# Optimization experiments

Measured on AMD Instinct MI355X. Metric: run time of the kernel, lower is better.

Reference implementation:

```python
import jax, jax.numpy as jnp
import numpy as np

# Problem sizes (batched graph of G molecules)
N = 100_000   # total nodes
E = 400_000   # total directed edges
G = 2_500     # number of molecule graphs
K = 3         # len(idx_wo_smiles) -> zero rows inserted
NODE_F = 74   # graph_feats_shape[0]
EDGE_F = 12   # graph_feats_shape[1]
HID = 128     # hidden_feats = dim // 2
DIM = 256     # dim


def setup_inputs() -> dict:
    key = jax.random.key(0)
    ks = jax.random.split(key, 20)
    init = lambda k, shape, fan: (jax.random.normal(k, shape, jnp.float32) / np.sqrt(fan)).astype(jnp.float32)

    node_feats = jax.random.normal(ks[0], (N, NODE_F), jnp.float32)
    edge_feats = jax.random.normal(ks[1], (E, EDGE_F), jnp.float32)  # passed but unused by GCN
    src = jax.random.randint(ks[2], (E,), 0, N)
    dst = jax.random.randint(ks[3], (E,), 0, N)
    # sorted graph ids, every graph non-empty (~40 atoms each)
    graph_ids = (jnp.arange(N) * G) // N
    idx_wo_smiles = jnp.arange(K)

    return {
        'node_feats': node_feats,
        'edge_feats': edge_feats,
        'W1': init(ks[4], (NODE_F, HID), NODE_F), 'b1': jnp.zeros((HID,), jnp.float32),
        'Wr1': init(ks[5], (NODE_F, HID), NODE_F), 'br1': jnp.zeros((HID,), jnp.float32),
        'W2': init(ks[6], (HID, HID), HID), 'b2': jnp.zeros((HID,), jnp.float32),
        'Wr2': init(ks[7], (HID, HID), HID), 'br2': jnp.zeros((HID,), jnp.float32),
        'w_atom': init(ks[8], (HID, 1), HID), 'b_atom': jnp.zeros((1,), jnp.float32),
        'Wp1': init(ks[9], (2 * HID, HID), 2 * HID), 'bp1': jnp.zeros((HID,), jnp.float32),
        'Wp2': init(ks[10], (HID, DIM), HID), 'bp2': jnp.zeros((DIM,), jnp.float32),
        'src': src, 'dst': dst, 'graph_ids': graph_ids, 'idx_wo_smiles': idx_wo_smiles,
    }


def reference(node_feats, edge_feats, W1, b1, Wr1, br1, W2, b2, Wr2, br2,
              w_atom, b_atom, Wp1, bp1, Wp2, bp2, src, dst, graph_ids, idx_wo_smiles):
    n = node_feats.shape[0]
    ones_e = jnp.ones(src.shape[0], jnp.float32)
    out_deg = jax.ops.segment_sum(ones_e, src, num_segments=n)
    in_deg = jax.ops.segment_sum(ones_e, dst, num_segments=n)
    norm_s = jax.lax.rsqrt(jnp.maximum(out_deg, 1.0))  # [N]
    norm_d = jax.lax.rsqrt(jnp.maximum(in_deg, 1.0))   # [N]

    def gcn_layer(h, W, b, Wr, br):
        # GraphConv(norm='both'): D^-1/2 A D^-1/2 h W + b, with relu activation
        m = h[src] * norm_s[src][:, None]                       # [E, F] gather
        agg = jax.ops.segment_sum(m, dst, num_segments=n)       # [N, F] scatter-add
        gc = jax.nn.relu((agg * norm_d[:, None]) @ W + b)
        res = jax.nn.relu(h @ Wr + br)                          # residual connection
        return gc + res

    h = gcn_layer(node_feats, W1, b1, Wr1, br1)   # [N, HID]
    h = gcn_layer(h, W2, b2, Wr2, br2)            # [N, HID]

    # WeightedSumAndMax readout per molecule
    aw = jax.nn.sigmoid(h @ w_atom + b_atom)                          # [N, 1]
    hsum = jax.ops.segment_sum(h * aw, graph_ids, num_segments=G)     # [G, HID]
    hmax = jax.ops.segment_max(h, graph_ids, num_segments=G)          # [G, HID]
    gfeat = jnp.concatenate([hsum, hmax], axis=1)                     # [G, 2*HID]

    latent = jax.nn.relu(gfeat @ Wp1 + bp1) @ Wp2 + bp2               # [G, DIM]

    # Insert zero rows at idx_wo_smiles (sorted ascending -> final positions)
    total = G + idx_wo_smiles.shape[0]
    zero_mask = jnp.zeros((total,), bool).at[idx_wo_smiles].set(True)
    keep = jnp.nonzero(~zero_mask, size=G)[0]
    out = jnp.zeros((total, latent.shape[1]), latent.dtype).at[keep].set(latent)
    return out
```

## Files before the change

kernel.cpp:

```cpp
#include <hip/hip_runtime.h>
#include <hip/hip_bf16.h>

#define NODE_F 74
#define HID 128
#define DIM 256

typedef __hip_bfloat16 bf16;
typedef unsigned int u32;
typedef unsigned short u16;

typedef short s16x8 __attribute__((ext_vector_type(8)));
typedef __bf16 bf16x8 __attribute__((ext_vector_type(8)));
typedef float f32x4 __attribute__((ext_vector_type(4)));

__device__ __forceinline__ float rdl(float v, int l){
  return __int_as_float(__builtin_amdgcn_readlane(__float_as_int(v), l));
}
__device__ __forceinline__ float2 bfpair(u32 u){
  float2 r;
  r.x = __uint_as_float(u << 16);
  r.y = __uint_as_float(u & 0xffff0000u);
  return r;
}
__device__ __forceinline__ u16 bfbits(float a){
  return __bfloat16_as_ushort(__float2bfloat16(a));
}

__global__ void k_deg(const int* __restrict__ src, const int* __restrict__ dst,
                      float* __restrict__ outdeg_f, int* __restrict__ indeg, int E_){
  int e = blockIdx.x*256 + threadIdx.x;
  if (e < E_){
    atomicAdd(&outdeg_f[src[e]], 1.0f);
    atomicAdd(&indeg[dst[e]], 1);
  }
}

__global__ __launch_bounds__(256) void k_scan_a(const int* __restrict__ indeg,
                                                float* __restrict__ norm_s,
                                                float* __restrict__ norm_d,
                                                int* __restrict__ bsum, int n){
  __shared__ int red[256];
  const int base = blockIdx.x*1024 + threadIdx.x*4;
  int s = 0;
  #pragma unroll
  for (int i = 0; i < 4; ++i){
    const int idx = base + i;
    if (idx < n){
      const int d = indeg[idx];
      s += d;
      norm_d[idx] = rsqrtf(fmaxf((float)d, 1.0f));
      norm_s[idx] = rsqrtf(fmaxf(norm_s[idx], 1.0f));
    }
  }
  red[threadIdx.x] = s;
  __syncthreads();
  #pragma unroll
  for (int off = 128; off; off >>= 1){
    if (threadIdx.x < off) red[threadIdx.x] += red[threadIdx.x + off];
    __syncthreads();
  }
  if (threadIdx.x == 0) bsum[blockIdx.x] = red[0];
}

__global__ __launch_bounds__(1024) void k_scan_b(int* __restrict__ bsum, int nb){
  __shared__ int part[1024];
  __shared__ int carry;
  if (threadIdx.x == 0) carry = 0;
  __syncthreads();
  for (int c0 = 0; c0 < nb; c0 += 1024){
    const int tid = threadIdx.x, idx = c0 + tid;
    part[tid] = (idx < nb) ? bsum[idx] : 0;
    __syncthreads();
    for (int off = 1; off < 1024; off <<= 1){
      const int t = (tid >= off) ? part[tid-off] : 0;
      __syncthreads();
      part[tid] += t;
      __syncthreads();
    }
    if (idx < nb) bsum[idx] = carry + ((tid == 0) ? 0 : part[tid-1]);
    __syncthreads();
    if (tid == 0) carry += part[1023];
    __syncthreads();
  }
}

__global__ __launch_bounds__(256) void k_scan_c(int* __restrict__ indeg,
                                                const int* __restrict__ bsum,
                                                int* __restrict__ row_ptr, int n){
  __shared__ int part[256];
  const int base = blockIdx.x*1024 + threadIdx.x*4;
  int v[4]; int s = 0;
  #pragma unroll
  for (int i = 0; i < 4; ++i){
    const int idx = base + i;
    v[i] = (idx < n) ? indeg[idx] : 0;
    s += v[i];
  }
  part[threadIdx.x] = s;
  __syncthreads();
  for (int off = 1; off < 256; off <<= 1){
    const int t = (threadIdx.x >= off) ? part[threadIdx.x-off] : 0;
    __syncthreads();
    part[threadIdx.x] += t;
    __syncthreads();
  }
  int run = bsum[blockIdx.x] + ((threadIdx.x == 0) ? 0 : part[threadIdx.x-1]);
  #pragma unroll
  for (int i = 0; i < 4; ++i){
    const int idx = base + i;
    if (idx < n){
      row_ptr[idx] = run;
      run += v[i];
      indeg[idx] = 0;
    }
    if (idx == n-1) row_ptr[n] = run;
  }
}

__global__ void k_fill(const int* __restrict__ src, const int* __restrict__ dst,
                       const int* __restrict__ row_ptr, int* __restrict__ cursor,
                       int* __restrict__ col, int E_){
  int e = blockIdx.x*256 + threadIdx.x;
  if (e < E_){
    int d = dst[e];
    int pos = row_ptr[d] + atomicAdd(&cursor[d], 1);
    col[pos] = src[e];
  }
}

__global__ __launch_bounds__(256) void k_prep_all(
    const float* __restrict__ W1, const float* __restrict__ Wr1,
    const float* __restrict__ W2, const float* __restrict__ Wr2,
    u16* __restrict__ Bp1, u16* __restrict__ Bp2){
  int idx = blockIdx.x*256 + threadIdx.x;
  const float* W; u16* dst; int S, Ktrue, loc;
  if      (idx < 12288){ W = W1;  dst = Bp1;          S = 3; Ktrue = NODE_F; loc = idx; }
  else if (idx < 24576){ W = Wr1; dst = Bp1 + 12288;  S = 3; Ktrue = NODE_F; loc = idx - 12288; }
  else if (idx < 40960){ W = W2;  dst = Bp2;          S = 4; Ktrue = HID;    loc = idx - 24576; }
  else if (idx < 57344){ W = Wr2; dst = Bp2 + 16384;  S = 4; Ktrue = HID;    loc = idx - 40960; }
  else return;
  const int e   = loc & 7;
  const int l   = (loc >> 3) & 63;
  const int rem = loc >> 9;
  const int s   = rem % S;
  const int t   = rem / S;
  const int k   = s*32 + (l >> 4)*8 + e;
  const int c   = t*16 + (l & 15);
  const float v = (k < Ktrue) ? W[(size_t)k*HID + c] : 0.f;
  dst[loc] = bfbits(v);
}

__global__ __launch_bounds__(256) void k_fgemm1(
    const float* __restrict__ x0, const int* __restrict__ row_ptr,
    const int* __restrict__ col, const float* __restrict__ norm_s,
    const float* __restrict__ norm_d,
    const u16* __restrict__ Bp, const float* __restrict__ bg_,
    const float* __restrict__ br_, u16* __restrict__ h1, int n){
  const int lane = threadIdx.x & 63;
  const int wid  = threadIdx.x >> 6;
  const int jg = lane & 15, kg = lane >> 4;
  const int r0 = blockIdx.x*64 + wid*16;
  const int row = r0 + jg;
  const bool rok = row < n;
  const int kb = kg*8;

  float agg[3][8];
  #pragma unroll
  for (int s = 0; s < 3; ++s)
    #pragma unroll
    for (int e = 0; e < 8; ++e) agg[s][e] = 0.f;

  auto accum = [&](const float* px, float ns){
    #pragma unroll
    for (int s = 0; s < 2; ++s){
      #pragma unroll
      for (int e = 0; e < 8; e += 2){
        const float2 v = *(const float2*)&px[s*32 + kb + e];
        agg[s][e]   = fmaf(v.x, ns, agg[s][e]);
        agg[s][e+1] = fmaf(v.y, ns, agg[s][e+1]);
      }
    }
    if (kg == 0){
      #pragma unroll
      for (int e = 0; e < 8; e += 2){
        const float2 v = *(const float2*)&px[64 + e];
        agg[2][e]   = fmaf(v.x, ns, agg[2][e]);
        agg[2][e+1] = fmaf(v.y, ns, agg[2][e+1]);
      }
    } else if (kg == 1){
      const float2 v = *(const float2*)&px[72];
      agg[2][0] = fmaf(v.x, ns, agg[2][0]);
      agg[2][1] = fmaf(v.y, ns, agg[2][1]);
    }
  };

  int p0 = 0, p1 = 0;
  if (rok){ p0 = row_ptr[row]; p1 = row_ptr[row+1]; }
  int p = p0;
  #pragma unroll 1
  for (; p + 3 < p1; p += 4){
    const int s0 = col[p], s1 = col[p+1], s2 = col[p+2], s3 = col[p+3];
    const float n0 = norm_s[s0], n1 = norm_s[s1], n2 = norm_s[s2], n3 = norm_s[s3];
    accum(x0 + (size_t)s0*NODE_F, n0);
    accum(x0 + (size_t)s1*NODE_F, n1);
    accum(x0 + (size_t)s2*NODE_F, n2);
    accum(x0 + (size_t)s3*NODE_F, n3);
  }
  #pragma unroll 1
  for (; p + 1 < p1; p += 2){
    const int s0 = col[p], s1 = col[p+1];
    const float n0 = norm_s[s0], n1 = norm_s[s1];
    accum(x0 + (size_t)s0*NODE_F, n0);
    accum(x0 + (size_t)s1*NODE_F, n1);
  }
  if (p < p1){
    const int s0 = col[p];
    accum(x0 + (size_t)s0*NODE_F, norm_s[s0]);
  }

  const float nd = rok ? norm_d[row] : 0.f;
  bf16x8 ag[3], ar[3];
  #pragma unroll
  for (int s = 0; s < 3; ++s)
    #pragma unroll
    for (int e = 0; e < 8; ++e) ag[s][e] = (__bf16)(agg[s][e]*nd);

  {
    const int rA = rok ? row : (n-1);
    const float* px = x0 + (size_t)rA*NODE_F;
    #pragma unroll
    for (int s = 0; s < 2; ++s)
      #pragma unroll
      for (int e = 0; e < 8; e += 2){
        const float2 w = *(const float2*)&px[s*32 + kb + e];
        ar[s][e]   = (__bf16)w.x;
        ar[s][e+1] = (__bf16)w.y;
      }
    #pragma unroll
    for (int e = 0; e < 8; ++e) ar[2][e] = (__bf16)0.f;
    if (kg == 0){
      #pragma unroll
      for (int e = 0; e < 8; e += 2){
        const float2 w = *(const float2*)&px[64 + e];
        ar[2][e]   = (__bf16)w.x;
        ar[2][e+1] = (__bf16)w.y;
      }
    } else if (kg == 1){
      const float2 w = *(const float2*)&px[72];
      ar[2][0] = (__bf16)w.x;
      ar[2][1] = (__bf16)w.y;
    }
  }

  f32x4 accg[8], accr[8];
  #pragma unroll
  for (int t = 0; t < 8; ++t){
    accg[t] = f32x4{0.f,0.f,0.f,0.f};
    accr[t] = f32x4{0.f,0.f,0.f,0.f};
  }
  constexpr int FR1 = 8*3*512;
  #pragma unroll
  for (int s = 0; s < 3; ++s){
    #pragma unroll
    for (int t = 0; t < 8; ++t){
      const bf16x8 bg = __builtin_bit_cast(bf16x8,
          *(const s16x8*)&Bp[((t*3 + s)*64 + lane)*8]);
      const bf16x8 br = __builtin_bit_cast(bf16x8,
          *(const s16x8*)&Bp[FR1 + ((t*3 + s)*64 + lane)*8]);
      accg[t] = __builtin_amdgcn_mfma_f32_16x16x32_bf16(ag[s], bg, accg[t], 0,0,0);
      accr[t] = __builtin_amdgcn_mfma_f32_16x16x32_bf16(ar[s], br, accr[t], 0,0,0);
    }
  }

  const int rowb = r0 + 4*kg;
  #pragma unroll
  for (int t = 0; t < 8; ++t){
    const int colc = t*16 + jg;
    const float bgv = bg_[colc], brv = br_[colc];
    #pragma unroll
    for (int r = 0; r < 4; ++r){
      const int row2 = rowb + r;
      if (row2 < n){
        const float o = fmaxf(accg[t][r] + bgv, 0.f) + fmaxf(accr[t][r] + brv, 0.f);
        h1[(size_t)row2*HID + colc] = bfbits(o);
      }
    }
  }
}

__global__ __launch_bounds__(256) void k_fgemm2(
    const u16* __restrict__ h1, const int* __restrict__ row_ptr,
    const int* __restrict__ col, const float* __restrict__ norm_s,
    const float* __restrict__ norm_d,
    const u16* __restrict__ Bp, const float* __restrict__ bg_,
    const float* __restrict__ br_,
    const float* __restrict__ w_atom, const float* __restrict__ b_atom,
    const int* __restrict__ gid,
    float* __restrict__ hsum, u32* __restrict__ hmax, int n){
  const int lane = threadIdx.x & 63;
  const int wid  = threadIdx.x >> 6;
  const int jg = lane & 15, kg = lane >> 4;
  const int r0 = blockIdx.x*64 + wid*16;
  const int row = r0 + jg;
  const bool rok = row < n;
  const int kb = kg*8;

  float agg[4][8];
  #pragma unroll
  for (int s = 0; s < 4; ++s)
    #pragma unroll
    for (int e = 0; e < 8; ++e) agg[s][e] = 0.f;

  auto accum = [&](uint4 v, int s, float ns){
    const float2 f0 = bfpair(v.x), f1 = bfpair(v.y);
    const float2 f2 = bfpair(v.z), f3 = bfpair(v.w);
    agg[s][0] = fmaf(f0.x, ns, agg[s][0]);
    agg[s][1] = fmaf(f0.y, ns, agg[s][1]);
    agg[s][2] = fmaf(f1.x, ns, agg[s][2]);
    agg[s][3] = fmaf(f1.y, ns, agg[s][3]);
    agg[s][4] = fmaf(f2.x, ns, agg[s][4]);
    agg[s][5] = fmaf(f2.y, ns, agg[s][5]);
    agg[s][6] = fmaf(f3.x, ns, agg[s][6]);
    agg[s][7] = fmaf(f3.y, ns, agg[s][7]);
  };
  auto gatherN = [&](const u16* ph, float ns){
    const uint4 v0 = *(const uint4*)(ph);
    const uint4 v1 = *(const uint4*)(ph + 32);
    const uint4 v2 = *(const uint4*)(ph + 64);
    const uint4 v3 = *(const uint4*)(ph + 96);
    accum(v0, 0, ns); accum(v1, 1, ns); accum(v2, 2, ns); accum(v3, 3, ns);
  };

  int p0 = 0, p1 = 0;
  if (rok){ p0 = row_ptr[row]; p1 = row_ptr[row+1]; }
  int p = p0;
  #pragma unroll 1
  for (; p + 3 < p1; p += 4){
    const int s0 = col[p], s1 = col[p+1], s2 = col[p+2], s3 = col[p+3];
    const float n0 = norm_s[s0], n1 = norm_s[s1], n2 = norm_s[s2], n3 = norm_s[s3];
    gatherN(h1 + (size_t)s0*HID + kb, n0);
    gatherN(h1 + (size_t)s1*HID + kb, n1);
    gatherN(h1 + (size_t)s2*HID + kb, n2);
    gatherN(h1 + (size_t)s3*HID + kb, n3);
  }
  #pragma unroll 1
  for (; p + 1 < p1; p += 2){
    const int s0 = col[p], s1 = col[p+1];
    const float n0 = norm_s[s0], n1 = norm_s[s1];
    gatherN(h1 + (size_t)s0*HID + kb, n0);
    gatherN(h1 + (size_t)s1*HID + kb, n1);
  }
  if (p < p1){
    const int s0 = col[p];
    gatherN(h1 + (size_t)s0*HID + kb, norm_s[s0]);
  }

  const float nd = rok ? norm_d[row] : 0.f;
  bf16x8 ag[4];
  #pragma unroll
  for (int s = 0; s < 4; ++s)
    #pragma unroll
    for (int e = 0; e < 8; ++e) ag[s][e] = (__bf16)(agg[s][e]*nd);

  const int rA = rok ? row : (n-1);
  const u16* phr = h1 + (size_t)rA*HID + kb;

  f32x4 accg[8], accr[8];
  #pragma unroll
  for (int t = 0; t < 8; ++t){
    accg[t] = f32x4{0.f,0.f,0.f,0.f};
    accr[t] = f32x4{0.f,0.f,0.f,0.f};
  }
  constexpr int FR2 = 8*4*512;
  #pragma unroll
  for (int s = 0; s < 4; ++s){
    const bf16x8 arf = __builtin_bit_cast(bf16x8, *(const s16x8*)(phr + s*32));
    #pragma unroll
    for (int t = 0; t < 8; ++t){
      const bf16x8 bg = __builtin_bit_cast(bf16x8,
          *(const s16x8*)&Bp[((t*4 + s)*64 + lane)*8]);
      const bf16x8 br = __builtin_bit_cast(bf16x8,
          *(const s16x8*)&Bp[FR2 + ((t*4 + s)*64 + lane)*8]);
      accg[t] = __builtin_amdgcn_mfma_f32_16x16x32_bf16(ag[s], bg, accg[t], 0,0,0);
      accr[t] = __builtin_amdgcn_mfma_f32_16x16x32_bf16(arf, br, accr[t], 0,0,0);
    }
  }

  float o[8][4];
  #pragma unroll
  for (int t = 0; t < 8; ++t){
    const int colc = t*16 + jg;
    const float bgv = bg_[colc], brv = br_[colc];
    #pragma unroll
    for (int r = 0; r < 4; ++r)
      o[t][r] = fmaxf(accg[t][r] + bgv, 0.f) + fmaxf(accr[t][r] + brv, 0.f);
  }
  if (r0 < n){
    float wa[8];
    #pragma unroll
    for (int t = 0; t < 8; ++t) wa[t] = w_atom[t*16 + jg];
    const float ba = b_atom[0];
    const int rowb = r0 + 4*kg;
    float awv[4]; int gidr[4];
    #pragma unroll
    for (int r = 0; r < 4; ++r){
      const int row2 = rowb + r;
      float dot = 0.f;
      #pragma unroll
      for (int t = 0; t < 8; ++t) dot = fmaf(o[t][r], wa[t], dot);
      dot += __shfl_xor(dot, 1);
      dot += __shfl_xor(dot, 2);
      dot += __shfl_xor(dot, 4);
      dot += __shfl_xor(dot, 8);
      awv[r]  = 1.0f/(1.0f + __expf(-(dot + ba)));
      gidr[r] = (row2 < n) ? gid[row2] : -1;
    }
    const int rhi    = (r0 + 15 < n) ? (r0 + 15) : (n - 1);
    const int gfirst = gid[r0];
    const int glast  = gid[rhi];
    for (int g = gfirst; g <= glast; ++g){
      #pragma unroll
      for (int t = 0; t < 8; ++t){
        float sv = 0.f, mv = 0.f;
        #pragma unroll
        for (int r = 0; r < 4; ++r){
          const bool in = (gidr[r] == g);
          sv += in ? o[t][r]*awv[r] : 0.f;
          mv  = in ? fmaxf(mv, o[t][r]) : mv;
        }
        sv += __shfl_xor(sv, 16);
        sv += __shfl_xor(sv, 32);
        mv  = fmaxf(mv, __shfl_xor(mv, 16));
        mv  = fmaxf(mv, __shfl_xor(mv, 32));
        if (lane < 16){
          atomicAdd(&hsum[(size_t)g*HID + t*16 + jg], sv);
          atomicMax(&hmax[(size_t)g*HID + t*16 + jg], __float_as_uint(mv));
        }
      }
    }
  }
}

__global__ __launch_bounds__(256) void k_mlp(
    const float* __restrict__ hsum, const float* __restrict__ hmaxf,
    const float* __restrict__ Wp1, const float* __restrict__ bp1,
    const float* __restrict__ Wp2, const float* __restrict__ bp2,
    const int* __restrict__ idxw, int K_,
    float* __restrict__ out, int G_){
  const int lane = threadIdx.x & 63;
  const int row = blockIdx.x*4 + (threadIdx.x >> 6);
  if (blockIdx.x == 0){
    for (int j = 0; j < K_; ++j){
      const int zr = idxw[j];
      for (int i = threadIdx.x; i < DIM; i += 256)
        out[(size_t)zr*DIM + i] = 0.f;
    }
  }
  if (row >= G_) return;
  const int c = lane*2;
  float ra0 = hsum [(size_t)row*HID + lane];
  float ra1 = hsum [(size_t)row*HID + 64 + lane];
  float ra2 = hmaxf[(size_t)row*HID + lane];
  float ra3 = hmaxf[(size_t)row*HID + 64 + lane];
  float a0 = 0.f, a1 = 0.f;
  #pragma unroll 4
  for (int k = 0; k < 64; ++k){
    const float v0 = rdl(ra0,k), v1 = rdl(ra1,k), v2 = rdl(ra2,k), v3 = rdl(ra3,k);
    const float2 w0 = *(const float2*)&Wp1[(size_t)(k      )*HID + c];
    const float2 w1 = *(const float2*)&Wp1[(size_t)(k +  64)*HID + c];
    const float2 w2 = *(const float2*)&Wp1[(size_t)(k + 128)*HID + c];
    const float2 w3 = *(const float2*)&Wp1[(size_t)(k + 192)*HID + c];
    a0 = fmaf(v0,w0.x, fmaf(v1,w1.x, fmaf(v2,w2.x, fmaf(v3,w3.x, a0))));
    a1 = fmaf(v0,w0.y, fmaf(v1,w1.y, fmaf(v2,w2.y, fmaf(v3,w3.y, a1))));
  }
  const float h0  = fmaxf(a0 + bp1[c],   0.f);
  const float h1v = fmaxf(a1 + bp1[c+1], 0.f);
  const int c4 = lane*4;
  float acc0=0.f, acc1=0.f, acc2=0.f, acc3=0.f;
  #pragma unroll 4
  for (int j = 0; j < 64; ++j){
    const float he = rdl(h0, j);
    const float ho = rdl(h1v, j);
    const float4 we = *(const float4*)&Wp2[(size_t)(2*j  )*DIM + c4];
    const float4 wo = *(const float4*)&Wp2[(size_t)(2*j+1)*DIM + c4];
    acc0 = fmaf(he,we.x, fmaf(ho,wo.x, acc0));
    acc1 = fmaf(he,we.y, fmaf(ho,wo.y, acc1));
    acc2 = fmaf(he,we.z, fmaf(ho,wo.z, acc2));
    acc3 = fmaf(he,we.w, fmaf(ho,wo.w, acc3));
  }
  int orow = row;
  for (int j = 0; j < K_; ++j){ if (idxw[j] <= orow) orow++; }
  float* po = out + (size_t)orow*DIM + c4;
  po[0] = acc0 + bp2[c4];
  po[1] = acc1 + bp2[c4+1];
  po[2] = acc2 + bp2[c4+2];
  po[3] = acc3 + bp2[c4+3];
}

extern "C" void kernel_launch(void* const* d_in, const int* in_sizes, int n_in,
                              void* d_out, int out_size, void* d_ws, size_t ws_size,
                              hipStream_t stream){
  (void)n_in; (void)ws_size;
  const float* x0     = (const float*)d_in[0];
  const float* W1     = (const float*)d_in[2];
  const float* b1     = (const float*)d_in[3];
  const float* Wr1    = (const float*)d_in[4];
  const float* br1    = (const float*)d_in[5];
  const float* W2     = (const float*)d_in[6];
  const float* b2     = (const float*)d_in[7];
  const float* Wr2    = (const float*)d_in[8];
  const float* br2    = (const float*)d_in[9];
  const float* w_atom = (const float*)d_in[10];
  const float* b_atom = (const float*)d_in[11];
  const float* Wp1    = (const float*)d_in[12];
  const float* bp1    = (const float*)d_in[13];
  const float* Wp2    = (const float*)d_in[14];
  const float* bp2    = (const float*)d_in[15];
  const int* src  = (const int*)d_in[16];
  const int* dst  = (const int*)d_in[17];
  const int* gid  = (const int*)d_in[18];
  const int* idxw = (const int*)d_in[19];

  const int N_ = in_sizes[0] / NODE_F;
  const int E_ = in_sizes[16];
  const int K_ = in_sizes[19];
  const int G_ = out_size / DIM - K_;

  u16*   h1     = (u16*)d_ws;
  float* norm_d = (float*)(h1 + (size_t)N_*HID);
  float* norm_s = norm_d + N_;
  float* hsum   = norm_s + N_;
  float* hmaxv  = hsum + (size_t)G_*HID;
  int*   indeg  = (int*)(hmaxv + (size_t)G_*HID);
  int*   row_ptr= indeg + N_;
  int*   col    = row_ptr + ((N_ + 4) & ~3);
  int*   bsum   = col + ((E_ + 4) & ~3);
  u16*   Bp1    = (u16*)d_out;
  u16*   Bp2    = Bp1 + 2*12288;

  hipMemsetAsync(norm_s, 0, ((size_t)2*N_ + (size_t)2*G_*HID)*sizeof(float), stream);

  const int nscan = (N_ + 1023)/1024;
  k_deg     <<<(E_+255)/256, 256, 0, stream>>>(src, dst, norm_s, indeg, E_);
  k_scan_a  <<<nscan, 256, 0, stream>>>(indeg, norm_s, norm_d, bsum, N_);
  k_scan_b  <<<1, 1024, 0, stream>>>(bsum, nscan);
  k_scan_c  <<<nscan, 256, 0, stream>>>(indeg, bsum, row_ptr, N_);
  k_fill    <<<(E_+255)/256, 256, 0, stream>>>(src, dst, row_ptr, indeg, col, E_);
  k_prep_all<<<(57344+255)/256, 256, 0, stream>>>(W1, Wr1, W2, Wr2, Bp1, Bp2);

  const int nb = (N_ + 63) / 64;
  k_fgemm1<<<nb, 256, 0, stream>>>(x0, row_ptr, col, norm_s, norm_d,
                                   Bp1, b1, br1, h1, N_);
  k_fgemm2<<<nb, 256, 0, stream>>>(h1, row_ptr, col, norm_s, norm_d,
                                   Bp2, b2, br2, w_atom, b_atom, gid,
                                   hsum, (u32*)hmaxv, N_);

  k_mlp<<<(G_+3)/4, 256, 0, stream>>>(hsum, hmaxv, Wp1, bp1, Wp2, bp2,
                                      idxw, K_, (float*)d_out, G_);
}
```

Before: 366.7 us.

## Split fused gather+GEMM layers into wavefront-per-row gather and separate MFMA GEMM kernels

```diff
diff --git a/kernel.cpp b/kernel.cpp
--- a/kernel.cpp
+++ b/kernel.cpp
@@ -1,5 +1,6 @@
 #include <hip/hip_runtime.h>
 #include <hip/hip_bf16.h>
+#include <stdint.h>
 
 #define NODE_F 74
 #define HID 128
@@ -21,6 +22,11 @@
   r.x = __uint_as_float(u << 16);
   r.y = __uint_as_float(u & 0xffff0000u);
   return r;
+}
+__device__ __forceinline__ u32 packbf(float a, float b){
+  u32 lo = (u32)__bfloat16_as_ushort(__float2bfloat16(a));
+  u32 hi = (u32)__bfloat16_as_ushort(__float2bfloat16(b));
+  return lo | (hi << 16);
 }
 __device__ __forceinline__ u16 bfbits(float a){
   return __bfloat16_as_ushort(__float2bfloat16(a));
@@ -150,6 +156,227 @@
   dst[loc] = bfbits(v);
 }
 
+__global__ __launch_bounds__(256) void k_gather1(
+    const float* __restrict__ x0, const int* __restrict__ row_ptr,
+    const int* __restrict__ col, const float* __restrict__ norm_s,
+    const float* __restrict__ norm_d, u32* __restrict__ ag1, int n){
+  const int lane = threadIdx.x & 63;
+  const int row  = blockIdx.x*4 + (threadIdx.x >> 6);
+  if (row >= n) return;
+  float a0 = 0.f, a1 = 0.f;
+  const int p0 = row_ptr[row], p1 = row_ptr[row+1];
+  const int c0 = 2*lane;
+  #pragma unroll 1
+  for (int p = p0; p < p1; ++p){
+    const int s = col[p];
+    const float ns = norm_s[s];
+    if (lane < 37){
+      const float2 v = *(const float2*)&x0[(size_t)s*NODE_F + c0];
+      a0 = fmaf(v.x, ns, a0);
+      a1 = fmaf(v.y, ns, a1);
+    }
+  }
+  if (lane < 48){
+    const float nd = norm_d[row];
+    ag1[(size_t)row*48 + lane] = packbf(a0*nd, a1*nd);
+  }
+}
+
+__global__ __launch_bounds__(256) void k_gather2(
+    const u32* __restrict__ h1u, const int* __restrict__ row_ptr,
+    const int* __restrict__ col, const float* __restrict__ norm_s,
+    const float* __restrict__ norm_d, u32* __restrict__ ag2, int n){
+  const int lane = threadIdx.x & 63;
+  const int row  = blockIdx.x*4 + (threadIdx.x >> 6);
+  if (row >= n) return;
+  float a0 = 0.f, a1 = 0.f;
+  const int p0 = row_ptr[row], p1 = row_ptr[row+1];
+  #pragma unroll 1
+  for (int p = p0; p < p1; ++p){
+    const int s = col[p];
+    const float ns = norm_s[s];
+    const float2 v = bfpair(h1u[(size_t)s*64 + lane]);
+    a0 = fmaf(v.x, ns, a0);
+    a1 = fmaf(v.y, ns, a1);
+  }
+  const float nd = norm_d[row];
+  ag2[(size_t)row*64 + lane] = packbf(a0*nd, a1*nd);
+}
+
+__global__ __launch_bounds__(256) void k_ggemm1(
+    const u16* __restrict__ ag1, const float* __restrict__ x0,
+    const u16* __restrict__ Bp, const float* __restrict__ bg_,
+    const float* __restrict__ br_, u16* __restrict__ h1, int n){
+  const int lane = threadIdx.x & 63;
+  const int wid  = threadIdx.x >> 6;
+  const int jg = lane & 15, kg = lane >> 4;
+  const int r0 = blockIdx.x*64 + wid*16;
+  const int row = r0 + jg;
+  const bool rok = row < n;
+  const int kb = kg*8;
+  const int rA = rok ? row : (n-1);
+
+  bf16x8 ag[3], ar[3];
+  #pragma unroll
+  for (int s = 0; s < 3; ++s)
+    ag[s] = __builtin_bit_cast(bf16x8, *(const s16x8*)&ag1[(size_t)rA*96 + s*32 + kb]);
+  {
+    const float* px = x0 + (size_t)rA*NODE_F;
+    #pragma unroll
+    for (int s = 0; s < 2; ++s)
+      #pragma unroll
+      for (int e = 0; e < 8; e += 2){
+        const float2 w = *(const float2*)&px[s*32 + kb + e];
+        ar[s][e]   = (__bf16)w.x;
+        ar[s][e+1] = (__bf16)w.y;
+      }
+    #pragma unroll
+    for (int e = 0; e < 8; ++e) ar[2][e] = (__bf16)0.f;
+    if (kg == 0){
+      #pragma unroll
+      for (int e = 0; e < 8; e += 2){
+        const float2 w = *(const float2*)&px[64 + e];
+        ar[2][e]   = (__bf16)w.x;
+        ar[2][e+1] = (__bf16)w.y;
+      }
+    } else if (kg == 1){
+      const float2 w = *(const float2*)&px[72];
+      ar[2][0] = (__bf16)w.x;
+      ar[2][1] = (__bf16)w.y;
+    }
+  }
+
+  f32x4 accg[8], accr[8];
+  #pragma unroll
+  for (int t = 0; t < 8; ++t){
+    accg[t] = f32x4{0.f,0.f,0.f,0.f};
+    accr[t] = f32x4{0.f,0.f,0.f,0.f};
+  }
+  constexpr int FR1 = 8*3*512;
+  #pragma unroll
+  for (int s = 0; s < 3; ++s){
+    #pragma unroll
+    for (int t = 0; t < 8; ++t){
+      const bf16x8 bg = __builtin_bit_cast(bf16x8,
+          *(const s16x8*)&Bp[((t*3 + s)*64 + lane)*8]);
+      const bf16x8 br = __builtin_bit_cast(bf16x8,
+          *(const s16x8*)&Bp[FR1 + ((t*3 + s)*64 + lane)*8]);
+      accg[t] = __builtin_amdgcn_mfma_f32_16x16x32_bf16(ag[s], bg, accg[t], 0,0,0);
+      accr[t] = __builtin_amdgcn_mfma_f32_16x16x32_bf16(ar[s], br, accr[t], 0,0,0);
+    }
+  }
+
+  const int rowb = r0 + 4*kg;
+  #pragma unroll
+  for (int t = 0; t < 8; ++t){
+    const int colc = t*16 + jg;
+    const float bgv = bg_[colc], brv = br_[colc];
+    #pragma unroll
+    for (int r = 0; r < 4; ++r){
+      const int row2 = rowb + r;
+      if (row2 < n){
+        const float o = fmaxf(accg[t][r] + bgv, 0.f) + fmaxf(accr[t][r] + brv, 0.f);
+        h1[(size_t)row2*HID + colc] = bfbits(o);
+      }
+    }
+  }
+}
+
+__global__ __launch_bounds__(256) void k_ggemm2(
+    const u16* __restrict__ ag2, const u16* __restrict__ h1,
+    const u16* __restrict__ Bp, const float* __restrict__ bg_,
+    const float* __restrict__ br_,
+    const float* __restrict__ w_atom, const float* __restrict__ b_atom,
+    const int* __restrict__ gid,
+    float* __restrict__ hsum, u32* __restrict__ hmax, int n){
+  const int lane = threadIdx.x & 63;
+  const int wid  = threadIdx.x >> 6;
+  const int jg = lane & 15, kg = lane >> 4;
+  const int r0 = blockIdx.x*64 + wid*16;
+  const int row = r0 + jg;
+  const bool rok = row < n;
+  const int kb = kg*8;
+  const int rA = rok ? row : (n-1);
+
+  f32x4 accg[8], accr[8];
+  #pragma unroll
+  for (int t = 0; t < 8; ++t){
+    accg[t] = f32x4{0.f,0.f,0.f,0.f};
+    accr[t] = f32x4{0.f,0.f,0.f,0.f};
+  }
+  constexpr int FR2 = 8*4*512;
+  #pragma unroll
+  for (int s = 0; s < 4; ++s){
+    const bf16x8 agf = __builtin_bit_cast(bf16x8,
+        *(const s16x8*)&ag2[(size_t)rA*HID + s*32 + kb]);
+    const bf16x8 arf = __builtin_bit_cast(bf16x8,
+        *(const s16x8*)&h1[(size_t)rA*HID + s*32 + kb]);
+    #pragma unroll
+    for (int t = 0; t < 8; ++t){
+      const bf16x8 bg = __builtin_bit_cast(bf16x8,
+          *(const s16x8*)&Bp[((t*4 + s)*64 + lane)*8]);
+      const bf16x8 br = __builtin_bit_cast(bf16x8,
+          *(const s16x8*)&Bp[FR2 + ((t*4 + s)*64 + lane)*8]);
+      accg[t] = __builtin_amdgcn_mfma_f32_16x16x32_bf16(agf, bg, accg[t], 0,0,0);
+      accr[t] = __builtin_amdgcn_mfma_f32_16x16x32_bf16(arf, br, accr[t], 0,0,0);
+    }
+  }
+
+  float o[8][4];
+  #pragma unroll
+  for (int t = 0; t < 8; ++t){
+    const int colc = t*16 + jg;
+    const float bgv = bg_[colc], brv = br_[colc];
+    #pragma unroll
+    for (int r = 0; r < 4; ++r)
+      o[t][r] = fmaxf(accg[t][r] + bgv, 0.f) + fmaxf(accr[t][r] + brv, 0.f);
+  }
+  if (r0 < n){
+    float wa[8];
+    #pragma unroll
+    for (int t = 0; t < 8; ++t) wa[t] = w_atom[t*16 + jg];
+    const float ba = b_atom[0];
+    const int rowb = r0 + 4*kg;
+    float awv[4]; int gidr[4];
+    #pragma unroll
+    for (int r = 0; r < 4; ++r){
+      const int row2 = rowb + r;
+      float dot = 0.f;
+      #pragma unroll
+      for (int t = 0; t < 8; ++t) dot = fmaf(o[t][r], wa[t], dot);
+      dot += __shfl_xor(dot, 1);
+      dot += __shfl_xor(dot, 2);
+      dot += __shfl_xor(dot, 4);
+      dot += __shfl_xor(dot, 8);
+      awv[r]  = 1.0f/(1.0f + __expf(-(dot + ba)));
+      gidr[r] = (row2 < n) ? gid[row2] : -1;
+    }
+    const int rhi    = (r0 + 15 < n) ? (r0 + 15) : (n - 1);
+    const int gfirst = gid[r0];
+    const int glast  = gid[rhi];
+    for (int g = gfirst; g <= glast; ++g){
+      #pragma unroll
+      for (int t = 0; t < 8; ++t){
+        float sv = 0.f, mv = 0.f;
+        #pragma unroll
+        for (int r = 0; r < 4; ++r){
+          const bool in = (gidr[r] == g);
+          sv += in ? o[t][r]*awv[r] : 0.f;
+          mv  = in ? fmaxf(mv, o[t][r]) : mv;
+        }
+        sv += __shfl_xor(sv, 16);
+        sv += __shfl_xor(sv, 32);
+        mv  = fmaxf(mv, __shfl_xor(mv, 16));
+        mv  = fmaxf(mv, __shfl_xor(mv, 32));
+        if (lane < 16){
+          atomicAdd(&hsum[(size_t)g*HID + t*16 + jg], sv);
+          atomicMax(&hmax[(size_t)g*HID + t*16 + jg], __float_as_uint(mv));
+        }
+      }
+    }
+  }
+}
+
 __global__ __launch_bounds__(256) void k_fgemm1(
     const float* __restrict__ x0, const int* __restrict__ row_ptr,
     const int* __restrict__ col, const float* __restrict__ norm_s,
@@ -197,15 +424,6 @@
   int p0 = 0, p1 = 0;
   if (rok){ p0 = row_ptr[row]; p1 = row_ptr[row+1]; }
   int p = p0;
-  #pragma unroll 1
-  for (; p + 3 < p1; p += 4){
-    const int s0 = col[p], s1 = col[p+1], s2 = col[p+2], s3 = col[p+3];
-    const float n0 = norm_s[s0], n1 = norm_s[s1], n2 = norm_s[s2], n3 = norm_s[s3];
-    accum(x0 + (size_t)s0*NODE_F, n0);
-    accum(x0 + (size_t)s1*NODE_F, n1);
-    accum(x0 + (size_t)s2*NODE_F, n2);
-    accum(x0 + (size_t)s3*NODE_F, n3);
-  }
   #pragma unroll 1
   for (; p + 1 < p1; p += 2){
     const int s0 = col[p], s1 = col[p+1];
@@ -335,15 +553,6 @@
   if (rok){ p0 = row_ptr[row]; p1 = row_ptr[row+1]; }
   int p = p0;
   #pragma unroll 1
-  for (; p + 3 < p1; p += 4){
-    const int s0 = col[p], s1 = col[p+1], s2 = col[p+2], s3 = col[p+3];
-    const float n0 = norm_s[s0], n1 = norm_s[s1], n2 = norm_s[s2], n3 = norm_s[s3];
-    gatherN(h1 + (size_t)s0*HID + kb, n0);
-    gatherN(h1 + (size_t)s1*HID + kb, n1);
-    gatherN(h1 + (size_t)s2*HID + kb, n2);
-    gatherN(h1 + (size_t)s3*HID + kb, n3);
-  }
-  #pragma unroll 1
   for (; p + 1 < p1; p += 2){
     const int s0 = col[p], s1 = col[p+1];
     const float n0 = norm_s[s0], n1 = norm_s[s1];
@@ -500,7 +709,7 @@
 extern "C" void kernel_launch(void* const* d_in, const int* in_sizes, int n_in,
                               void* d_out, int out_size, void* d_ws, size_t ws_size,
                               hipStream_t stream){
-  (void)n_in; (void)ws_size;
+  (void)n_in;
   const float* x0     = (const float*)d_in[0];
   const float* W1     = (const float*)d_in[2];
   const float* b1     = (const float*)d_in[3];
@@ -535,12 +744,17 @@
   int*   row_ptr= indeg + N_;
   int*   col    = row_ptr + ((N_ + 4) & ~3);
   int*   bsum   = col + ((E_ + 4) & ~3);
+  const int nscan = (N_ + 1023)/1024;
+  uintptr_t aggp = ((uintptr_t)(bsum + nscan) + 255) & ~(uintptr_t)255;
+  u32* aggu = (u32*)aggp;
+  const size_t need_split = (aggp + (size_t)N_*64*sizeof(u32)) - (uintptr_t)d_ws;
+  const bool use_split = (ws_size >= need_split);
+
   u16*   Bp1    = (u16*)d_out;
   u16*   Bp2    = Bp1 + 2*12288;
 
   hipMemsetAsync(norm_s, 0, ((size_t)2*N_ + (size_t)2*G_*HID)*sizeof(float), stream);
 
-  const int nscan = (N_ + 1023)/1024;
   k_deg     <<<(E_+255)/256, 256, 0, stream>>>(src, dst, norm_s, indeg, E_);
   k_scan_a  <<<nscan, 256, 0, stream>>>(indeg, norm_s, norm_d, bsum, N_);
   k_scan_b  <<<1, 1024, 0, stream>>>(bsum, nscan);
@@ -548,12 +762,22 @@
   k_fill    <<<(E_+255)/256, 256, 0, stream>>>(src, dst, row_ptr, indeg, col, E_);
   k_prep_all<<<(57344+255)/256, 256, 0, stream>>>(W1, Wr1, W2, Wr2, Bp1, Bp2);
 
-  const int nb = (N_ + 63) / 64;
-  k_fgemm1<<<nb, 256, 0, stream>>>(x0, row_ptr, col, norm_s, norm_d,
-                                   Bp1, b1, br1, h1, N_);
-  k_fgemm2<<<nb, 256, 0, stream>>>(h1, row_ptr, col, norm_s, norm_d,
-                                   Bp2, b2, br2, w_atom, b_atom, gid,
-                                   hsum, (u32*)hmaxv, N_);
+  const int nb  = (N_ + 63) / 64;
+  const int nbw = (N_ + 3) / 4;
+  if (use_split){
+    k_gather1<<<nbw, 256, 0, stream>>>(x0, row_ptr, col, norm_s, norm_d, aggu, N_);
+    k_ggemm1 <<<nb, 256, 0, stream>>>((const u16*)aggu, x0, Bp1, b1, br1, h1, N_);
+    k_gather2<<<nbw, 256, 0, stream>>>((const u32*)h1, row_ptr, col, norm_s, norm_d,
+                                       aggu, N_);
+    k_ggemm2 <<<nb, 256, 0, stream>>>((const u16*)aggu, h1, Bp2, b2, br2,
+                                      w_atom, b_atom, gid, hsum, (u32*)hmaxv, N_);
+  } else {
+    k_fgemm1<<<nb, 256, 0, stream>>>(x0, row_ptr, col, norm_s, norm_d,
+                                     Bp1, b1, br1, h1, N_);
+    k_fgemm2<<<nb, 256, 0, stream>>>(h1, row_ptr, col, norm_s, norm_d,
+                                     Bp2, b2, br2, w_atom, b_atom, gid,
+                                     hsum, (u32*)hmaxv, N_);
+  }
 
   k_mlp<<<(G_+3)/4, 256, 0, stream>>>(hsum, hmaxv, Wp1, bp1, Wp2, bp2,
                                       idxw, K_, (float*)d_out, G_);
```

Measured after the change: 411.7 us. 12.3% more time.

## Split fused gather+GEMM into wave-per-row gather kernels and separate MFMA GEMMs

Applied to the files above, without the earlier changes.

```diff
diff --git a/kernel.cpp b/kernel.cpp
--- a/kernel.cpp
+++ b/kernel.cpp
@@ -1,5 +1,6 @@
 #include <hip/hip_runtime.h>
 #include <hip/hip_bf16.h>
+#include <stdint.h>
 
 #define NODE_F 74
 #define HID 128
@@ -22,16 +23,41 @@
   r.y = __uint_as_float(u & 0xffff0000u);
   return r;
 }
+__device__ __forceinline__ u32 packbf(float a, float b){
+  u32 lo = (u32)__bfloat16_as_ushort(__float2bfloat16(a));
+  u32 hi = (u32)__bfloat16_as_ushort(__float2bfloat16(b));
+  return lo | (hi << 16);
+}
 __device__ __forceinline__ u16 bfbits(float a){
   return __bfloat16_as_ushort(__float2bfloat16(a));
 }
 
-__global__ void k_deg(const int* __restrict__ src, const int* __restrict__ dst,
-                      float* __restrict__ outdeg_f, int* __restrict__ indeg, int E_){
+__global__ void k_deg_prep(const int* __restrict__ src, const int* __restrict__ dst_,
+                           float* __restrict__ outdeg_f, int* __restrict__ indeg, int E_,
+                           const float* __restrict__ W1, const float* __restrict__ Wr1,
+                           const float* __restrict__ W2, const float* __restrict__ Wr2,
+                           u16* __restrict__ Bp1, u16* __restrict__ Bp2){
   int e = blockIdx.x*256 + threadIdx.x;
   if (e < E_){
     atomicAdd(&outdeg_f[src[e]], 1.0f);
-    atomicAdd(&indeg[dst[e]], 1);
+    atomicAdd(&indeg[dst_[e]], 1);
+  }
+  int idx = e;
+  if (idx < 57344){
+    const float* W; u16* dstp; int S, Ktrue, loc;
+    if      (idx < 12288){ W = W1;  dstp = Bp1;          S = 3; Ktrue = NODE_F; loc = idx; }
+    else if (idx < 24576){ W = Wr1; dstp = Bp1 + 12288;  S = 3; Ktrue = NODE_F; loc = idx - 12288; }
+    else if (idx < 40960){ W = W2;  dstp = Bp2;          S = 4; Ktrue = HID;    loc = idx - 24576; }
+    else                 { W = Wr2; dstp = Bp2 + 16384;  S = 4; Ktrue = HID;    loc = idx - 40960; }
+    const int el  = loc & 7;
+    const int l   = (loc >> 3) & 63;
+    const int rem = loc >> 9;
+    const int s   = rem % S;
+    const int t   = rem / S;
+    const int k   = s*32 + (l >> 4)*8 + el;
+    const int c   = t*16 + (l & 15);
+    const float v = (k < Ktrue) ? W[(size_t)k*HID + c] : 0.f;
+    dstp[loc] = bfbits(v);
   }
 }
 
@@ -128,32 +154,99 @@
   }
 }
 
-__global__ __launch_bounds__(256) void k_prep_all(
-    const float* __restrict__ W1, const float* __restrict__ Wr1,
-    const float* __restrict__ W2, const float* __restrict__ Wr2,
-    u16* __restrict__ Bp1, u16* __restrict__ Bp2){
-  int idx = blockIdx.x*256 + threadIdx.x;
-  const float* W; u16* dst; int S, Ktrue, loc;
-  if      (idx < 12288){ W = W1;  dst = Bp1;          S = 3; Ktrue = NODE_F; loc = idx; }
-  else if (idx < 24576){ W = Wr1; dst = Bp1 + 12288;  S = 3; Ktrue = NODE_F; loc = idx - 12288; }
-  else if (idx < 40960){ W = W2;  dst = Bp2;          S = 4; Ktrue = HID;    loc = idx - 24576; }
-  else if (idx < 57344){ W = Wr2; dst = Bp2 + 16384;  S = 4; Ktrue = HID;    loc = idx - 40960; }
-  else return;
-  const int e   = loc & 7;
-  const int l   = (loc >> 3) & 63;
-  const int rem = loc >> 9;
-  const int s   = rem % S;
-  const int t   = rem / S;
-  const int k   = s*32 + (l >> 4)*8 + e;
-  const int c   = t*16 + (l & 15);
-  const float v = (k < Ktrue) ? W[(size_t)k*HID + c] : 0.f;
-  dst[loc] = bfbits(v);
-}
-
-__global__ __launch_bounds__(256) void k_fgemm1(
+__global__ __launch_bounds__(256) void k_gather1(
     const float* __restrict__ x0, const int* __restrict__ row_ptr,
     const int* __restrict__ col, const float* __restrict__ norm_s,
-    const float* __restrict__ norm_d,
+    const float* __restrict__ norm_d, u32* __restrict__ ag1, int n){
+  const int lane = threadIdx.x & 63;
+  const int row  = blockIdx.x*4 + (threadIdx.x >> 6);
+  if (row >= n) return;
+  const int p0 = row_ptr[row], p1 = row_ptr[row+1];
+  const bool act = (lane < 37);
+  const float* xb = x0 + 2*lane;
+  float a0 = 0.f, a1 = 0.f;
+  int p = p0;
+  #pragma unroll 1
+  for (; p + 3 < p1; p += 4){
+    const int s0 = col[p], s1 = col[p+1], s2 = col[p+2], s3 = col[p+3];
+    const float n0 = norm_s[s0], n1 = norm_s[s1], n2 = norm_s[s2], n3 = norm_s[s3];
+    float2 v0{0.f,0.f}, v1{0.f,0.f}, v2{0.f,0.f}, v3{0.f,0.f};
+    if (act){
+      v0 = *(const float2*)&xb[(size_t)s0*NODE_F];
+      v1 = *(const float2*)&xb[(size_t)s1*NODE_F];
+      v2 = *(const float2*)&xb[(size_t)s2*NODE_F];
+      v3 = *(const float2*)&xb[(size_t)s3*NODE_F];
+    }
+    a0 = fmaf(v0.x,n0, fmaf(v1.x,n1, fmaf(v2.x,n2, fmaf(v3.x,n3, a0))));
+    a1 = fmaf(v0.y,n0, fmaf(v1.y,n1, fmaf(v2.y,n2, fmaf(v3.y,n3, a1))));
+  }
+  const int rem = p1 - p;
+  if (rem > 0){
+    const int s0 = col[p];
+    int s1 = s0, s2 = s0;
+    float n1 = 0.f, n2 = 0.f;
+    const float n0 = norm_s[s0];
+    if (rem > 1){ s1 = col[p+1]; n1 = norm_s[s1]; }
+    if (rem > 2){ s2 = col[p+2]; n2 = norm_s[s2]; }
+    float2 v0{0.f,0.f}, v1{0.f,0.f}, v2{0.f,0.f};
+    if (act){
+      v0 = *(const float2*)&xb[(size_t)s0*NODE_F];
+      v1 = *(const float2*)&xb[(size_t)s1*NODE_F];
+      v2 = *(const float2*)&xb[(size_t)s2*NODE_F];
+    }
+    a0 = fmaf(v0.x,n0, fmaf(v1.x,n1, fmaf(v2.x,n2, a0)));
+    a1 = fmaf(v0.y,n0, fmaf(v1.y,n1, fmaf(v2.y,n2, a1)));
+  }
+  if (lane < 48){
+    const float nd = norm_d[row];
+    ag1[(size_t)row*48 + lane] = packbf(a0*nd, a1*nd);
+  }
+}
+
+__global__ __launch_bounds__(256) void k_gather2(
+    const u32* __restrict__ h1u, const int* __restrict__ row_ptr,
+    const int* __restrict__ col, const float* __restrict__ norm_s,
+    const float* __restrict__ norm_d, u32* __restrict__ ag2, int n){
+  const int lane = threadIdx.x & 63;
+  const int row  = blockIdx.x*4 + (threadIdx.x >> 6);
+  if (row >= n) return;
+  const int p0 = row_ptr[row], p1 = row_ptr[row+1];
+  const u32* hb = h1u + lane;
+  float a0 = 0.f, a1 = 0.f;
+  int p = p0;
+  #pragma unroll 1
+  for (; p + 3 < p1; p += 4){
+    const int s0 = col[p], s1 = col[p+1], s2 = col[p+2], s3 = col[p+3];
+    const float n0 = norm_s[s0], n1 = norm_s[s1], n2 = norm_s[s2], n3 = norm_s[s3];
+    const u32 u0 = hb[(size_t)s0*64];
+    const u32 u1 = hb[(size_t)s1*64];
+    const u32 u2 = hb[(size_t)s2*64];
+    const u32 u3 = hb[(size_t)s3*64];
+    const float2 f0 = bfpair(u0), f1 = bfpair(u1), f2 = bfpair(u2), f3 = bfpair(u3);
+    a0 = fmaf(f0.x,n0, fmaf(f1.x,n1, fmaf(f2.x,n2, fmaf(f3.x,n3, a0))));
+    a1 = fmaf(f0.y,n0, fmaf(f1.y,n1, fmaf(f2.y,n2, fmaf(f3.y,n3, a1))));
+  }
+  const int rem = p1 - p;
+  if (rem > 0){
+    const int s0 = col[p];
+    int s1 = s0, s2 = s0;
+    float n1 = 0.f, n2 = 0.f;
+    const float n0 = norm_s[s0];
+    if (rem > 1){ s1 = col[p+1]; n1 = norm_s[s1]; }
+    if (rem > 2){ s2 = col[p+2]; n2 = norm_s[s2]; }
+    const u32 u0 = hb[(size_t)s0*64];
+    const u32 u1 = hb[(size_t)s1*64];
+    const u32 u2 = hb[(size_t)s2*64];
+    const float2 f0 = bfpair(u0), f1 = bfpair(u1), f2 = bfpair(u2);
+    a0 = fmaf(f0.x,n0, fmaf(f1.x,n1, fmaf(f2.x,n2, a0)));
+    a1 = fmaf(f0.y,n0, fmaf(f1.y,n1, fmaf(f2.y,n2, a1)));
+  }
+  const float nd = norm_d[row];
+  ag2[(size_t)row*64 + lane] = packbf(a0*nd, a1*nd);
+}
+
+__global__ __launch_bounds__(256) void k_ggemm1(
+    const u16* __restrict__ ag1, const float* __restrict__ x0,
     const u16* __restrict__ Bp, const float* __restrict__ bg_,
     const float* __restrict__ br_, u16* __restrict__ h1, int n){
   const int lane = threadIdx.x & 63;
@@ -163,70 +256,13 @@
   const int row = r0 + jg;
   const bool rok = row < n;
   const int kb = kg*8;
-
-  float agg[3][8];
+  const int rA = rok ? row : (n-1);
+
+  bf16x8 ag[3], ar[3];
   #pragma unroll
   for (int s = 0; s < 3; ++s)
-    #pragma unroll
-    for (int e = 0; e < 8; ++e) agg[s][e] = 0.f;
-
-  auto accum = [&](const float* px, float ns){
-    #pragma unroll
-    for (int s = 0; s < 2; ++s){
-      #pragma unroll
-      for (int e = 0; e < 8; e += 2){
-        const float2 v = *(const float2*)&px[s*32 + kb + e];
-        agg[s][e]   = fmaf(v.x, ns, agg[s][e]);
-        agg[s][e+1] = fmaf(v.y, ns, agg[s][e+1]);
-      }
-    }
-    if (kg == 0){
-      #pragma unroll
-      for (int e = 0; e < 8; e += 2){
-        const float2 v = *(const float2*)&px[64 + e];
-        agg[2][e]   = fmaf(v.x, ns, agg[2][e]);
-        agg[2][e+1] = fmaf(v.y, ns, agg[2][e+1]);
-      }
-    } else if (kg == 1){
-      const float2 v = *(const float2*)&px[72];
-      agg[2][0] = fmaf(v.x, ns, agg[2][0]);
-      agg[2][1] = fmaf(v.y, ns, agg[2][1]);
-    }
-  };
-
-  int p0 = 0, p1 = 0;
-  if (rok){ p0 = row_ptr[row]; p1 = row_ptr[row+1]; }
-  int p = p0;
-  #pragma unroll 1
-  for (; p + 3 < p1; p += 4){
-    const int s0 = col[p], s1 = col[p+1], s2 = col[p+2], s3 = col[p+3];
-    const float n0 = norm_s[s0], n1 = norm_s[s1], n2 = norm_s[s2], n3 = norm_s[s3];
-    accum(x0 + (size_t)s0*NODE_F, n0);
-    accum(x0 + (size_t)s1*NODE_F, n1);
-    accum(x0 + (size_t)s2*NODE_F, n2);
-    accum(x0 + (size_t)s3*NODE_F, n3);
-  }
-  #pragma unroll 1
-  for (; p + 1 < p1; p += 2){
-    const int s0 = col[p], s1 = col[p+1];
-    const float n0 = norm_s[s0], n1 = norm_s[s1];
-    accum(x0 + (size_t)s0*NODE_F, n0);
-    accum(x0 + (size_t)s1*NODE_F, n1);
-  }
-  if (p < p1){
-    const int s0 = col[p];
-    accum(x0 + (size_t)s0*NODE_F, norm_s[s0]);
-  }
-
-  const float nd = rok ? norm_d[row] : 0.f;
-  bf16x8 ag[3], ar[3];
-  #pragma unroll
-  for (int s = 0; s < 3; ++s)
-    #pragma unroll
-    for (int e = 0; e < 8; ++e) ag[s][e] = (__bf16)(agg[s][e]*nd);
-
+    ag[s] = __builtin_bit_cast(bf16x8, *(const s16x8*)&ag1[(size_t)rA*96 + s*32 + kb]);
   {
-    const int rA = rok ? row : (n-1);
     const float* px = x0 + (size_t)rA*NODE_F;
     #pragma unroll
     for (int s = 0; s < 2; ++s)
@@ -288,10 +324,8 @@
   }
 }
 
-__global__ __launch_bounds__(256) void k_fgemm2(
-    const u16* __restrict__ h1, const int* __restrict__ row_ptr,
-    const int* __restrict__ col, const float* __restrict__ norm_s,
-    const float* __restrict__ norm_d,
+__global__ __launch_bounds__(256) void k_ggemm2(
+    const u16* __restrict__ ag2, const u16* __restrict__ h1,
     const u16* __restrict__ Bp, const float* __restrict__ bg_,
     const float* __restrict__ br_,
     const float* __restrict__ w_atom, const float* __restrict__ b_atom,
@@ -304,66 +338,7 @@
   const int row = r0 + jg;
   const bool rok = row < n;
   const int kb = kg*8;
-
-  float agg[4][8];
-  #pragma unroll
-  for (int s = 0; s < 4; ++s)
-    #pragma unroll
-    for (int e = 0; e < 8; ++e) agg[s][e] = 0.f;
-
-  auto accum = [&](uint4 v, int s, float ns){
-    const float2 f0 = bfpair(v.x), f1 = bfpair(v.y);
-    const float2 f2 = bfpair(v.z), f3 = bfpair(v.w);
-    agg[s][0] = fmaf(f0.x, ns, agg[s][0]);
-    agg[s][1] = fmaf(f0.y, ns, agg[s][1]);
-    agg[s][2] = fmaf(f1.x, ns, agg[s][2]);
-    agg[s][3] = fmaf(f1.y, ns, agg[s][3]);
-    agg[s][4] = fmaf(f2.x, ns, agg[s][4]);
-    agg[s][5] = fmaf(f2.y, ns, agg[s][5]);
-    agg[s][6] = fmaf(f3.x, ns, agg[s][6]);
-    agg[s][7] = fmaf(f3.y, ns, agg[s][7]);
-  };
-  auto gatherN = [&](const u16* ph, float ns){
-    const uint4 v0 = *(const uint4*)(ph);
-    const uint4 v1 = *(const uint4*)(ph + 32);
-    const uint4 v2 = *(const uint4*)(ph + 64);
-    const uint4 v3 = *(const uint4*)(ph + 96);
-    accum(v0, 0, ns); accum(v1, 1, ns); accum(v2, 2, ns); accum(v3, 3, ns);
-  };
-
-  int p0 = 0, p1 = 0;
-  if (rok){ p0 = row_ptr[row]; p1 = row_ptr[row+1]; }
-  int p = p0;
-  #pragma unroll 1
-  for (; p + 3 < p1; p += 4){
-    const int s0 = col[p], s1 = col[p+1], s2 = col[p+2], s3 = col[p+3];
-    const float n0 = norm_s[s0], n1 = norm_s[s1], n2 = norm_s[s2], n3 = norm_s[s3];
-    gatherN(h1 + (size_t)s0*HID + kb, n0);
-    gatherN(h1 + (size_t)s1*HID + kb, n1);
-    gatherN(h1 + (size_t)s2*HID + kb, n2);
-    gatherN(h1 + (size_t)s3*HID + kb, n3);
-  }
-  #pragma unroll 1
-  for (; p + 1 < p1; p += 2){
-    const int s0 = col[p], s1 = col[p+1];
-    const float n0 = norm_s[s0], n1 = norm_s[s1];
-    gatherN(h1 + (size_t)s0*HID + kb, n0);
-    gatherN(h1 + (size_t)s1*HID + kb, n1);
-  }
-  if (p < p1){
-    const int s0 = col[p];
-    gatherN(h1 + (size_t)s0*HID + kb, norm_s[s0]);
-  }
-
-  const float nd = rok ? norm_d[row] : 0.f;
-  bf16x8 ag[4];
-  #pragma unroll
-  for (int s = 0; s < 4; ++s)
-    #pragma unroll
-    for (int e = 0; e < 8; ++e) ag[s][e] = (__bf16)(agg[s][e]*nd);
-
   const int rA = rok ? row : (n-1);
-  const u16* phr = h1 + (size_t)rA*HID + kb;
 
   f32x4 accg[8], accr[8];
   #pragma unroll
@@ -374,14 +349,17 @@
   constexpr int FR2 = 8*4*512;
   #pragma unroll
   for (int s = 0; s < 4; ++s){
-    const bf16x8 arf = __builtin_bit_cast(bf16x8, *(const s16x8*)(phr + s*32));
+    const bf16x8 agf = __builtin_bit_cast(bf16x8,
+        *(const s16x8*)&ag2[(size_t)rA*HID + s*32 + kb]);
+    const bf16x8 arf = __builtin_bit_cast(bf16x8,
+        *(const s16x8*)&h1[(size_t)rA*HID + s*32 + kb]);
     #pragma unroll
     for (int t = 0; t < 8; ++t){
       const bf16x8 bg = __builtin_bit_cast(bf16x8,
           *(const s16x8*)&Bp[((t*4 + s)*64 + lane)*8]);
       const bf16x8 br = __builtin_bit_cast(bf16x8,
           *(const s16x8*)&Bp[FR2 + ((t*4 + s)*64 + lane)*8]);
-      accg[t] = __builtin_amdgcn_mfma_f32_16x16x32_bf16(ag[s], bg, accg[t], 0,0,0);
+      accg[t] = __builtin_amdgcn_mfma_f32_16x16x32_bf16(agf, bg, accg[t], 0,0,0);
       accr[t] = __builtin_amdgcn_mfma_f32_16x16x32_bf16(arf, br, accr[t], 0,0,0);
     }
   }
@@ -535,25 +513,30 @@
   int*   row_ptr= indeg + N_;
   int*   col    = row_ptr + ((N_ + 4) & ~3);
   int*   bsum   = col + ((E_ + 4) & ~3);
+  const int nscan = (N_ + 1023)/1024;
+  uintptr_t aggp = ((uintptr_t)(bsum + nscan) + 255) & ~(uintptr_t)255;
+  u32* aggu = (u32*)aggp;
+
   u16*   Bp1    = (u16*)d_out;
   u16*   Bp2    = Bp1 + 2*12288;
 
   hipMemsetAsync(norm_s, 0, ((size_t)2*N_ + (size_t)2*G_*HID)*sizeof(float), stream);
 
-  const int nscan = (N_ + 1023)/1024;
-  k_deg     <<<(E_+255)/256, 256, 0, stream>>>(src, dst, norm_s, indeg, E_);
+  k_deg_prep<<<(E_+255)/256, 256, 0, stream>>>(src, dst, norm_s, indeg, E_,
+                                               W1, Wr1, W2, Wr2, Bp1, Bp2);
   k_scan_a  <<<nscan, 256, 0, stream>>>(indeg, norm_s, norm_d, bsum, N_);
   k_scan_b  <<<1, 1024, 0, stream>>>(bsum, nscan);
   k_scan_c  <<<nscan, 256, 0, stream>>>(indeg, bsum, row_ptr, N_);
   k_fill    <<<(E_+255)/256, 256, 0, stream>>>(src, dst, row_ptr, indeg, col, E_);
-  k_prep_all<<<(57344+255)/256, 256, 0, stream>>>(W1, Wr1, W2, Wr2, Bp1, Bp2);
-
-  const int nb = (N_ + 63) / 64;
-  k_fgemm1<<<nb, 256, 0, stream>>>(x0, row_ptr, col, norm_s, norm_d,
-                                   Bp1, b1, br1, h1, N_);
-  k_fgemm2<<<nb, 256, 0, stream>>>(h1, row_ptr, col, norm_s, norm_d,
-                                   Bp2, b2, br2, w_atom, b_atom, gid,
-                                   hsum, (u32*)hmaxv, N_);
+
+  const int nb  = (N_ + 63) / 64;
+  const int nbw = (N_ + 3) / 4;
+  k_gather1<<<nbw, 256, 0, stream>>>(x0, row_ptr, col, norm_s, norm_d, aggu, N_);
+  k_ggemm1 <<<nb, 256, 0, stream>>>((const u16*)aggu, x0, Bp1, b1, br1, h1, N_);
+  k_gather2<<<nbw, 256, 0, stream>>>((const u32*)h1, row_ptr, col, norm_s, norm_d,
+                                     aggu, N_);
+  k_ggemm2 <<<nb, 256, 0, stream>>>((const u16*)aggu, h1, Bp2, b2, br2,
+                                    w_atom, b_atom, gid, hsum, (u32*)hmaxv, N_);
 
   k_mlp<<<(G_+3)/4, 256, 0, stream>>>(hsum, hmaxv, Wp1, bp1, Wp2, bp2,
                                       idxw, K_, (float*)d_out, G_);
```

After: 373.9 us. No clear change (+2.0%).
